# Optimization experiments

Hardware: AMD Instinct MI355X
Metric: run time of the kernel (lower is better)

Reference implementation:

```python
import jax, jax.numpy as jnp
import numpy as np

TEMPERATURE = 0.1
N, D = 8192, 1024

def setup_inputs() -> dict:
    key = jax.random.key(0)
    k1, k2 = jax.random.split(key)
    im = jax.random.normal(k1, (N, D), dtype=jnp.float32)
    cap = jax.random.normal(k2, (N, D), dtype=jnp.float32)
    return {"im": im, "cap": cap}

def reference(im, cap):
    # InfoNCE (info_nce package) L2-normalizes query, positive and negatives.
    # Per-sample loop: for image i, positive = cap[i], negatives = cap[j != i].
    # Logits set = sim(im_i, cap_j) for all j, positive at j == i, so
    # loss_i = logsumexp_j(S[i, j] / T) - S[i, i] / T  (CLIP-style CE).
    imn = im / jnp.linalg.norm(im, axis=-1, keepdims=True)
    capn = cap / jnp.linalg.norm(cap, axis=-1, keepdims=True)
    S = jnp.einsum('id,jd->ij', imn, capn) / TEMPERATURE  # [N, N]
    diag = jnp.diagonal(S)
    loss_i2c = jax.nn.logsumexp(S, axis=1) - diag  # image -> caption direction
    loss_c2i = jax.nn.logsumexp(S, axis=0) - diag  # caption -> image direction
    # original averages all 2N per-sample losses
    return 0.5 * (jnp.mean(loss_i2c) + jnp.mean(loss_c2i))
```

## Files before the change

### kernel.cpp

```cpp
#include <hip/hip_runtime.h>
#include <stdint.h>

#define N_ 8192
#define D_ 1024
#define EPILOGUE_SCALE (10.0f / 256.0f)
#define ENC_SCALE 16.0f
#define SLAB 262144

typedef float f32x4 __attribute__((ext_vector_type(4)));

#define GLD16(gsrc, ldst)                                                    \
  __builtin_amdgcn_global_load_lds(                                          \
      (const __attribute__((address_space(1))) unsigned int*)(gsrc),         \
      (__attribute__((address_space(3))) unsigned int*)(ldst), 16, 0, 0)


__global__ __launch_bounds__(1024) void normalize_k(
    const float* __restrict__ im, const float* __restrict__ cap,
    unsigned int* __restrict__ imn, unsigned int* __restrict__ capn,
    float* __restrict__ diag, float* __restrict__ sums ) {
  __shared__ unsigned int ldsA[16 * 257];
  __shared__ unsigned int ldsB[16 * 257];
  const int til = blockIdx.x;
  const int t = threadIdx.x;
  if (til < 4) ((float4*)sums)[til * 1024 + t] = (float4){0.f, 0.f, 0.f, 0.f};

  const int r = t >> 6, j = t & 63;
  const int row = til * 16 + r;
  const float4* __restrict__ aR = (const float4*)(im + (size_t)row * D_);
  const float4* __restrict__ bR = (const float4*)(cap + (size_t)row * D_);

  float4 a0 = aR[j], a1 = aR[j + 64], a2 = aR[j + 128], a3 = aR[j + 192];
  float4 b0 = bR[j], b1 = bR[j + 64], b2 = bR[j + 128], b3 = bR[j + 192];

  float ssa = a0.x * a0.x + a0.y * a0.y + a0.z * a0.z + a0.w * a0.w
            + a1.x * a1.x + a1.y * a1.y + a1.z * a1.z + a1.w * a1.w
            + a2.x * a2.x + a2.y * a2.y + a2.z * a2.z + a2.w * a2.w
            + a3.x * a3.x + a3.y * a3.y + a3.z * a3.z + a3.w * a3.w;
  float ssb = b0.x * b0.x + b0.y * b0.y + b0.z * b0.z + b0.w * b0.w
            + b1.x * b1.x + b1.y * b1.y + b1.z * b1.z + b1.w * b1.w
            + b2.x * b2.x + b2.y * b2.y + b2.z * b2.z + b2.w * b2.w
            + b3.x * b3.x + b3.y * b3.y + b3.z * b3.z + b3.w * b3.w;
  float dt  = a0.x * b0.x + a0.y * b0.y + a0.z * b0.z + a0.w * b0.w
            + a1.x * b1.x + a1.y * b1.y + a1.z * b1.z + a1.w * b1.w
            + a2.x * b2.x + a2.y * b2.y + a2.z * b2.z + a2.w * b2.w
            + a3.x * b3.x + a3.y * b3.y + a3.z * b3.z + a3.w * b3.w;
#pragma unroll
  for (int o = 1; o < 64; o <<= 1) {
    ssa += __shfl_xor(ssa, o, 64);
    ssb += __shfl_xor(ssb, o, 64);
    dt  += __shfl_xor(dt, o, 64);
  }
  const float ra = rsqrtf(ssa), rb = rsqrtf(ssb);
  if (j == 0) diag[row] = dt * ra * rb * 10.0f;
  const float sa = ra * ENC_SCALE, sb = rb * ENC_SCALE;

#define CVT_ST(av, bv, ofs)                                                  \
  {                                                                          \
    int pa_ = __builtin_amdgcn_cvt_pk_fp8_f32(av.x * sa, av.y * sa, 0, false); \
    pa_ = __builtin_amdgcn_cvt_pk_fp8_f32(av.z * sa, av.w * sa, pa_, true);  \
    int pb_ = __builtin_amdgcn_cvt_pk_fp8_f32(bv.x * sb, bv.y * sb, 0, false); \
    pb_ = __builtin_amdgcn_cvt_pk_fp8_f32(bv.z * sb, bv.w * sb, pb_, true);  \
    ldsA[r * 257 + j + (ofs)] = (unsigned int)pa_;                           \
    ldsB[r * 257 + j + (ofs)] = (unsigned int)pb_;                           \
  }
  CVT_ST(a0, b0, 0)
  CVT_ST(a1, b1, 64)
  CVT_ST(a2, b2, 128)
  CVT_ST(a3, b3, 192)
#undef CVT_ST
  __syncthreads();

  {
    const int s = t >> 5, c4 = t & 31;
    const int fl0 = c4 * 2, fl1 = fl0 + 1;
    const int i0 = (fl0 & 15) * 257 + s * 8 + (fl0 >> 4) * 2;
    const int i1 = (fl1 & 15) * 257 + s * 8 + (fl1 >> 4) * 2;
    uint4 va, vb;
    va.x = ldsA[i0]; va.y = ldsA[i0 + 1];
    va.z = ldsA[i1]; va.w = ldsA[i1 + 1];
    vb.x = ldsB[i0]; vb.y = ldsB[i0 + 1];
    vb.z = ldsB[i1]; vb.w = ldsB[i1 + 1];
    const size_t d = (size_t)s * 65536 + (size_t)til * 128 + c4 * 4;
    *(uint4*)(imn + d) = va;
    *(uint4*)(capn + d) = vb;
  }
}

__global__ __launch_bounds__(512, 4) void gemm_lse_k(
    const unsigned char* __restrict__ A,
    const unsigned char* __restrict__ B,
    float* __restrict__ rowsum, float* __restrict__ colsum) {
  __shared__ unsigned char lds[2][24576];
  const int t = threadIdx.x;
  const int w = t >> 6, l = t & 63;

  const int bid = blockIdx.x + (blockIdx.y << 5);
  const int nid = (bid & 7) * 256 + (bid >> 3);
  const int rowT = ((nid >> 8) << 2) + (nid & 3);
  const int colT = (nid >> 2) & 63;

  const size_t baseA = (size_t)rowT * 8192;
  const size_t baseB = (size_t)colT * 4096;

  const unsigned char* src[3];
  int ldsOff[3];
#pragma unroll
  for (int c = 0; c < 3; ++c) {
    const int o = w * 3072 + c * 1024;
    ldsOff[c] = o;
    if (o < 16384)
      src[c] = A + baseA + (size_t)(o >> 13) * SLAB + (o & 8191) + l * 16;
    else {
      const int ob = o - 16384;
      src[c] = B + baseB + (size_t)(ob >> 12) * SLAB + (ob & 4095) + l * 16;
    }
  }

#define STAGE(ktv, buf)                                                      \
  {                                                                          \
    const size_t kofs = (size_t)(ktv) * (2 * (size_t)SLAB);                  \
    GLD16(src[0] + kofs, &lds[buf][ldsOff[0]]);                              \
    GLD16(src[1] + kofs, &lds[buf][ldsOff[1]]);                              \
    GLD16(src[2] + kofs, &lds[buf][ldsOff[2]]);                              \
  }

  const int wr = w >> 1, wc = w & 1;
  const int aoff = wr * 2048 + l * 8;
  const int boff = wc * 2048 + l * 8;

  f32x4 acc[4][4];
#pragma unroll
  for (int m = 0; m < 4; ++m)
#pragma unroll
    for (int n = 0; n < 4; ++n) acc[m][n] = (f32x4){0.f, 0.f, 0.f, 0.f};

#define COMPUTE(buf)                                                         \
  {                                                                          \
    const unsigned char* Lc = &lds[buf][0];                                  \
    _Pragma("unroll")                                                        \
    for (int si = 0; si < 2; ++si) {                                         \
      long a_[4], b_[4];                                                     \
      _Pragma("unroll")                                                      \
      for (int m = 0; m < 4; ++m)                                            \
        a_[m] = *(const long*)(Lc + si * 8192 + aoff + m * 512);             \
      _Pragma("unroll")                                                      \
      for (int n = 0; n < 4; ++n)                                            \
        b_[n] = *(const long*)(Lc + 16384 + si * 4096 + boff + n * 512);     \
      _Pragma("unroll")                                                      \
      for (int m = 0; m < 4; ++m)                                            \
        _Pragma("unroll")                                                    \
        for (int n = 0; n < 4; ++n)                                          \
          acc[m][n] = __builtin_amdgcn_mfma_f32_16x16x32_fp8_fp8(            \
              a_[m], b_[n], acc[m][n], 0, 0, 0);                             \
    }                                                                        \
  }

  STAGE(0, 0)

#pragma unroll 1
  for (int kt = 0; kt < 15; ++kt) {
    STAGE(kt + 1, (kt + 1) & 1)
    asm volatile("s_waitcnt vmcnt(3)" ::: "memory");
    __builtin_amdgcn_s_barrier();
    COMPUTE(kt & 1)
    __builtin_amdgcn_s_barrier();
  }
  asm volatile("s_waitcnt vmcnt(0)" ::: "memory");
  __builtin_amdgcn_s_barrier();
  COMPUTE(1)
#undef COMPUTE
#undef STAGE

#pragma unroll
  for (int m = 0; m < 4; ++m)
#pragma unroll
    for (int n = 0; n < 4; ++n)
#pragma unroll
      for (int r = 0; r < 4; ++r)
        acc[m][n][r] = __expf(acc[m][n][r] * EPILOGUE_SCALE);

  const int rowBase = rowT * 256 + wr * 64;
  const int colBase = colT * 128 + wc * 64;
#pragma unroll
  for (int m = 0; m < 4; ++m)
#pragma unroll
    for (int r = 0; r < 4; ++r) {
      float v = 0.f;
#pragma unroll
      for (int n = 0; n < 4; ++n) v += acc[m][n][r];
      v += __shfl_xor(v, 1, 64);
      v += __shfl_xor(v, 2, 64);
      v += __shfl_xor(v, 4, 64);
      v += __shfl_xor(v, 8, 64);
      if ((l & 15) == 0)
        atomicAdd(&rowsum[rowBase + m * 16 + (l >> 4) * 4 + r], v);
    }
#pragma unroll
  for (int n = 0; n < 4; ++n) {
    float v = 0.f;
#pragma unroll
    for (int m = 0; m < 4; ++m)
      v += acc[m][n][0] + acc[m][n][1] + acc[m][n][2] + acc[m][n][3];
    v += __shfl_xor(v, 16, 64);
    v += __shfl_xor(v, 32, 64);
    if (l < 16)
      atomicAdd(&colsum[colBase + n * 16 + l], v);
  }
}

__global__ __launch_bounds__(256) void finalize_k(
    const float* __restrict__ rowsum, const float* __restrict__ colsum,
    const float* __restrict__ diag, float* __restrict__ out) {
  const int t = threadIdx.x;
  float lse = 0.f, dg = 0.f;
  for (int i = t; i < N_; i += 256) {
    lse += __logf(rowsum[i]) + __logf(colsum[i]);
    dg += diag[i];
  }
#pragma unroll
  for (int o = 32; o > 0; o >>= 1) {
    lse += __shfl_down(lse, o, 64);
    dg  += __shfl_down(dg, o, 64);
  }
  __shared__ float red[2][4];
  const int w = t >> 6, l = t & 63;
  if (l == 0) { red[0][w] = lse; red[1][w] = dg; }
  __syncthreads();
  if (t == 0) {
    lse = red[0][0] + red[0][1] + red[0][2] + red[0][3];
    dg  = red[1][0] + red[1][1] + red[1][2] + red[1][3];
    out[0] = 0.5f * lse / (float)N_ - dg / (float)N_;
  }
}

extern "C" void kernel_launch(void* const* d_in, const int* in_sizes, int n_in,
                              void* d_out, int out_size, void* d_ws, size_t ws_size,
                              hipStream_t stream) {
  const float* im = (const float*)d_in[0];
  const float* cap = (const float*)d_in[1];
  float* out = (float*)d_out;
  char* ws = (char*)d_ws;
  unsigned char* imn = (unsigned char*)ws;
  unsigned char* capn = imn + (size_t)N_ * D_;
  float* rowsum = (float*)(ws + 2 * (size_t)N_ * D_);
  float* colsum = rowsum + N_;
  float* diag = colsum + N_;

  normalize_k<<<512, 1024, 0, stream>>>(im, cap, (unsigned int*)imn,
                                        (unsigned int*)capn, diag, rowsum);
  gemm_lse_k<<<dim3(32, 64), 512, 0, stream>>>(imn, capn, rowsum, colsum);
  finalize_k<<<1, 256, 0, stream>>>(rowsum, colsum, diag, out);
}
```

Measured before the change: 193.5 us.

## Switch fp8 GEMM to 32x32x64 scaled MFMA with matching operand layout

Replaces the 16x16x32 fp8 MFMA with the gfx950 mfma_scale 32x32x64 f8f6f4 instruction using neutral scales. The normalize kernel now writes fp8 data in a new chunked layout, so each lane reads 16-byte runs that feed the 32-wide K operand directly. The epilogue reductions are rewritten for the 32x32 accumulator layout. The aim is fewer MFMA issues and wider, fewer LDS reads per K step. The cost is a larger accumulator register footprint per instruction and index mapping that must be exactly right.

```diff
diff --git a/kernel.cpp b/kernel.cpp
--- a/kernel.cpp
+++ b/kernel.cpp
@@ -5,9 +5,12 @@
 #define D_ 1024
 #define EPILOGUE_SCALE (10.0f / 256.0f)
 #define ENC_SCALE 16.0f
-#define SLAB 262144
+#define CHUNK 524288
 
 typedef float f32x4 __attribute__((ext_vector_type(4)));
+typedef float f32x16 __attribute__((ext_vector_type(16)));
+typedef int i32x4 __attribute__((ext_vector_type(4)));
+typedef int i32x8 __attribute__((ext_vector_type(8)));
 
 #define GLD16(gsrc, ldst)                                                    \
   __builtin_amdgcn_global_load_lds(                                          \
@@ -19,8 +22,8 @@
     const float* __restrict__ im, const float* __restrict__ cap,
     unsigned int* __restrict__ imn, unsigned int* __restrict__ capn,
     float* __restrict__ diag, float* __restrict__ sums ) {
-  __shared__ unsigned int ldsA[16 * 257];
-  __shared__ unsigned int ldsB[16 * 257];
+  __shared__ unsigned int ldsA[16 * 260];
+  __shared__ unsigned int ldsB[16 * 260];
   const int til = blockIdx.x;
   const int t = threadIdx.x;
   if (til < 4) ((float4*)sums)[til * 1024 + t] = (float4){0.f, 0.f, 0.f, 0.f};
@@ -61,8 +64,8 @@
     pa_ = __builtin_amdgcn_cvt_pk_fp8_f32(av.z * sa, av.w * sa, pa_, true);  \
     int pb_ = __builtin_amdgcn_cvt_pk_fp8_f32(bv.x * sb, bv.y * sb, 0, false); \
     pb_ = __builtin_amdgcn_cvt_pk_fp8_f32(bv.z * sb, bv.w * sb, pb_, true);  \
-    ldsA[r * 257 + j + (ofs)] = (unsigned int)pa_;                           \
-    ldsB[r * 257 + j + (ofs)] = (unsigned int)pb_;                           \
+    ldsA[r * 260 + j + (ofs)] = (unsigned int)pa_;                           \
+    ldsB[r * 260 + j + (ofs)] = (unsigned int)pb_;                           \
   }
   CVT_ST(a0, b0, 0)
   CVT_ST(a1, b1, 64)
@@ -72,18 +75,15 @@
   __syncthreads();
 
   {
-    const int s = t >> 5, c4 = t & 31;
-    const int fl0 = c4 * 2, fl1 = fl0 + 1;
-    const int i0 = (fl0 & 15) * 257 + s * 8 + (fl0 >> 4) * 2;
-    const int i1 = (fl1 & 15) * 257 + s * 8 + (fl1 >> 4) * 2;
-    uint4 va, vb;
-    va.x = ldsA[i0]; va.y = ldsA[i0 + 1];
-    va.z = ldsA[i1]; va.w = ldsA[i1 + 1];
-    vb.x = ldsB[i0]; vb.y = ldsB[i0 + 1];
-    vb.z = ldsB[i1]; vb.w = ldsB[i1 + 1];
-    const size_t d = (size_t)s * 65536 + (size_t)til * 128 + c4 * 4;
-    *(uint4*)(imn + d) = va;
-    *(uint4*)(capn + d) = vb;
+    const int q = t >> 4, rp = t & 15;
+    const uint4 va = *(const uint4*)&ldsA[rp * 260 + q * 4];
+    const uint4 vb = *(const uint4*)&ldsB[rp * 260 + q * 4];
+    const int row32 = ((til & 1) << 4) + rp;
+    const size_t d = (size_t)(q >> 2) * CHUNK + (size_t)(til >> 1) * 2048
+                   + (size_t)((q & 1) << 10)
+                   + (size_t)((((q >> 1) & 1) << 5) + row32) * 16;
+    *(uint4*)((unsigned char*)imn + d) = va;
+    *(uint4*)((unsigned char*)capn + d) = vb;
   }
 }
 
@@ -94,14 +94,15 @@
   __shared__ unsigned char lds[2][24576];
   const int t = threadIdx.x;
   const int w = t >> 6, l = t & 63;
+  const int l16 = l * 16;
 
   const int bid = blockIdx.x + (blockIdx.y << 5);
   const int nid = (bid & 7) * 256 + (bid >> 3);
   const int rowT = ((nid >> 8) << 2) + (nid & 3);
   const int colT = (nid >> 2) & 63;
 
-  const size_t baseA = (size_t)rowT * 8192;
-  const size_t baseB = (size_t)colT * 4096;
+  const size_t baseA = (size_t)rowT * 16384;
+  const size_t baseB = (size_t)colT * 8192;
 
   const unsigned char* src[3];
   int ldsOff[3];
@@ -109,51 +110,50 @@
   for (int c = 0; c < 3; ++c) {
     const int o = w * 3072 + c * 1024;
     ldsOff[c] = o;
-    if (o < 16384)
-      src[c] = A + baseA + (size_t)(o >> 13) * SLAB + (o & 8191) + l * 16;
-    else {
-      const int ob = o - 16384;
-      src[c] = B + baseB + (size_t)(ob >> 12) * SLAB + (ob & 4095) + l * 16;
-    }
-  }
-
-#define STAGE(ktv, buf)                                                      \
+    src[c] = (o < 16384) ? (A + baseA + o + l16)
+                         : (B + baseB + (o - 16384) + l16);
+  }
+
+#define STAGE(kc, buf)                                                       \
   {                                                                          \
-    const size_t kofs = (size_t)(ktv) * (2 * (size_t)SLAB);                  \
+    const size_t kofs = (size_t)(kc) * CHUNK;                                \
     GLD16(src[0] + kofs, &lds[buf][ldsOff[0]]);                              \
     GLD16(src[1] + kofs, &lds[buf][ldsOff[1]]);                              \
     GLD16(src[2] + kofs, &lds[buf][ldsOff[2]]);                              \
   }
 
   const int wr = w >> 1, wc = w & 1;
-  const int aoff = wr * 2048 + l * 8;
-  const int boff = wc * 2048 + l * 8;
-
-  f32x4 acc[4][4];
-#pragma unroll
-  for (int m = 0; m < 4; ++m)
-#pragma unroll
-    for (int n = 0; n < 4; ++n) acc[m][n] = (f32x4){0.f, 0.f, 0.f, 0.f};
+
+  f32x16 acc[2][2];
+#pragma unroll
+  for (int m = 0; m < 2; ++m)
+#pragma unroll
+    for (int n = 0; n < 2; ++n)
+#pragma unroll
+      for (int r = 0; r < 16; ++r) acc[m][n][r] = 0.f;
 
 #define COMPUTE(buf)                                                         \
   {                                                                          \
     const unsigned char* Lc = &lds[buf][0];                                  \
+    i32x8 a_[2], b_[2];                                                      \
     _Pragma("unroll")                                                        \
-    for (int si = 0; si < 2; ++si) {                                         \
-      long a_[4], b_[4];                                                     \
+    for (int m = 0; m < 2; ++m) {                                            \
+      i32x4 lo = *(const i32x4*)(Lc + (wr * 2 + m) * 2048 + l16);            \
+      i32x4 hi = *(const i32x4*)(Lc + (wr * 2 + m) * 2048 + 1024 + l16);     \
+      a_[m] = __builtin_shufflevector(lo, hi, 0, 1, 2, 3, 4, 5, 6, 7);       \
+    }                                                                        \
+    _Pragma("unroll")                                                        \
+    for (int n = 0; n < 2; ++n) {                                            \
+      i32x4 lo = *(const i32x4*)(Lc + 16384 + (wc * 2 + n) * 2048 + l16);    \
+      i32x4 hi = *(const i32x4*)(Lc + 16384 + (wc * 2 + n) * 2048 + 1024 + l16); \
+      b_[n] = __builtin_shufflevector(lo, hi, 0, 1, 2, 3, 4, 5, 6, 7);       \
+    }                                                                        \
+    _Pragma("unroll")                                                        \
+    for (int m = 0; m < 2; ++m)                                              \
       _Pragma("unroll")                                                      \
-      for (int m = 0; m < 4; ++m)                                            \
-        a_[m] = *(const long*)(Lc + si * 8192 + aoff + m * 512);             \
-      _Pragma("unroll")                                                      \
-      for (int n = 0; n < 4; ++n)                                            \
-        b_[n] = *(const long*)(Lc + 16384 + si * 4096 + boff + n * 512);     \
-      _Pragma("unroll")                                                      \
-      for (int m = 0; m < 4; ++m)                                            \
-        _Pragma("unroll")                                                    \
-        for (int n = 0; n < 4; ++n)                                          \
-          acc[m][n] = __builtin_amdgcn_mfma_f32_16x16x32_fp8_fp8(            \
-              a_[m], b_[n], acc[m][n], 0, 0, 0);                             \
-    }                                                                        \
+      for (int n = 0; n < 2; ++n)                                            \
+        acc[m][n] = __builtin_amdgcn_mfma_scale_f32_32x32x64_f8f6f4(         \
+            a_[m], b_[n], acc[m][n], 0, 0, 0, 0x7F7F7F7F, 0, 0x7F7F7F7F);    \
   }
 
   STAGE(0, 0)
@@ -173,39 +173,38 @@
 #undef STAGE
 
 #pragma unroll
-  for (int m = 0; m < 4; ++m)
-#pragma unroll
-    for (int n = 0; n < 4; ++n)
-#pragma unroll
-      for (int r = 0; r < 4; ++r)
+  for (int m = 0; m < 2; ++m)
+#pragma unroll
+    for (int n = 0; n < 2; ++n)
+#pragma unroll
+      for (int r = 0; r < 16; ++r)
         acc[m][n][r] = __expf(acc[m][n][r] * EPILOGUE_SCALE);
 
   const int rowBase = rowT * 256 + wr * 64;
   const int colBase = colT * 128 + wc * 64;
 #pragma unroll
-  for (int m = 0; m < 4; ++m)
-#pragma unroll
-    for (int r = 0; r < 4; ++r) {
-      float v = 0.f;
-#pragma unroll
-      for (int n = 0; n < 4; ++n) v += acc[m][n][r];
+  for (int m = 0; m < 2; ++m) {
+    f32x16 s = acc[m][0] + acc[m][1];
+#pragma unroll
+    for (int r = 0; r < 16; ++r) {
+      float v = s[r];
       v += __shfl_xor(v, 1, 64);
       v += __shfl_xor(v, 2, 64);
       v += __shfl_xor(v, 4, 64);
       v += __shfl_xor(v, 8, 64);
-      if ((l & 15) == 0)
-        atomicAdd(&rowsum[rowBase + m * 16 + (l >> 4) * 4 + r], v);
+      v += __shfl_xor(v, 16, 64);
+      if ((l & 31) == 0)
+        atomicAdd(&rowsum[rowBase + m * 32 + (r & 3) + 8 * (r >> 2) + 4 * (l >> 5)], v);
     }
-#pragma unroll
-  for (int n = 0; n < 4; ++n) {
+  }
+#pragma unroll
+  for (int n = 0; n < 2; ++n) {
     float v = 0.f;
 #pragma unroll
-    for (int m = 0; m < 4; ++m)
-      v += acc[m][n][0] + acc[m][n][1] + acc[m][n][2] + acc[m][n][3];
-    v += __shfl_xor(v, 16, 64);
+    for (int r = 0; r < 16; ++r) v += acc[0][n][r] + acc[1][n][r];
     v += __shfl_xor(v, 32, 64);
-    if (l < 16)
-      atomicAdd(&colsum[colBase + n * 16 + l], v);
+    if (l < 32)
+      atomicAdd(&colsum[colBase + n * 32 + l], v);
   }
 }
 
```

Result: no change. 196.1 us (+1.4%).
